# Kernel tuning notes

Measured on AMD Instinct MI355X. Metric: run time of the kernel, lower is better.

Reference implementation:

```python
import jax, jax.numpy as jnp
import numpy as np

N = 50000      # nodes
E = 800000     # edges (before self-loops)
F_IN = 128     # num_features
HID = 32       # hidden_channels
HEADS = 4
CLS = 40       # num_classes
NEG_SLOPE = 0.2


def setup_inputs() -> dict:
    key = jax.random.key(0)
    ks = jax.random.split(key, 10)
    s = 0.1
    x = jax.random.normal(ks[0], (N, F_IN), jnp.float32)
    edge_index = jax.random.randint(ks[1], (2, E), 0, N, jnp.int32)
    W1 = jax.random.normal(ks[2], (F_IN, HEADS * HID), jnp.float32) * s
    att_src1 = jax.random.normal(ks[3], (HEADS, HID), jnp.float32) * s
    att_dst1 = jax.random.normal(ks[4], (HEADS, HID), jnp.float32) * s
    b1 = jnp.zeros((HEADS * HID,), jnp.float32)
    W2 = jax.random.normal(ks[5], (HEADS * HID, CLS), jnp.float32) * s
    att_src2 = jax.random.normal(ks[6], (1, CLS), jnp.float32) * s
    att_dst2 = jax.random.normal(ks[7], (1, CLS), jnp.float32) * s
    b2 = jnp.zeros((CLS,), jnp.float32)
    return {"x": x, "edge_index": edge_index,
            "W1": W1, "att_src1": att_src1, "att_dst1": att_dst1, "b1": b1,
            "W2": W2, "att_src2": att_src2, "att_dst2": att_dst2, "b2": b2}


def gat_layer(x, src, dst, W, a_src, a_dst, b, concat):
    """PyG GATConv: per-head linear, edge attention logits a_src.h_j + a_dst.h_i,
    LeakyReLU, segment softmax over incoming edges per dst, weighted scatter-sum."""
    n = x.shape[0]
    H, C = a_src.shape
    h = (x @ W).reshape(n, H, C)                       # [N, H, C]
    al_s = jnp.einsum('nhc,hc->nh', h, a_src)          # [N, H]
    al_d = jnp.einsum('nhc,hc->nh', h, a_dst)          # [N, H]
    e = jax.nn.leaky_relu(al_s[src] + al_d[dst], NEG_SLOPE)  # [E, H]
    e_max = jax.lax.stop_gradient(jax.ops.segment_max(e, dst, num_segments=n))
    e = jnp.exp(e - e_max[dst])
    denom = jax.ops.segment_sum(e, dst, num_segments=n)      # [N, H]
    alpha = e / (denom[dst] + 1e-16)                         # [E, H]
    out = jax.ops.segment_sum(h[src] * alpha[:, :, None], dst, num_segments=n)  # [N, H, C]
    out = out.reshape(n, H * C) if concat else out.mean(axis=1)
    return out + b


def reference(x, edge_index, W1, att_src1, att_dst1, b1, W2, att_src2, att_dst2, b2):
    n = x.shape[0]
    loops = jnp.arange(n, dtype=edge_index.dtype)
    src = jnp.concatenate([edge_index[0], loops])  # PyG adds self-loops by default
    dst = jnp.concatenate([edge_index[1], loops])
    h = gat_layer(x, src, dst, W1, att_src1, att_dst1, b1, concat=True)
    h = jax.nn.relu(h)  # dropout is identity in eval mode
    h = gat_layer(h, src, dst, W2, att_src2, att_dst2, b2, concat=False)
    return jax.nn.log_softmax(h, axis=1)
```

## Files before the change

### kernel.cpp

```cpp
#include <hip/hip_runtime.h>
#include <hip/hip_bf16.h>
#include <cstdint>
#include <cstddef>

#define NN 50000
#define EE 800000
#define ETOT (EE + NN)
#define FIN 128
#define D1 128
#define HEADS 4
#define HID 32
#define CLS 40
#define NEG 0.2f
#define MAXDEG 64
#define NPART 8
#define PSIZE 6250
#define GB 79
#define BGB (NPART * GB)

typedef __attribute__((ext_vector_type(8))) short short8;
typedef __attribute__((ext_vector_type(4))) float float4v;

union U16 { uint4 u; short8 s; };

__device__ __forceinline__ float bf2f(unsigned short u) {
    union { unsigned int i; float f; } v; v.i = ((unsigned int)u) << 16; return v.f;
}
__device__ __forceinline__ unsigned short f2bf(float f) {
    union { unsigned int i; float f; } v; v.f = f;
    unsigned int r = v.i + 0x7fffu + ((v.i >> 16) & 1u);
    return (unsigned short)(r >> 16);
}

__global__ __launch_bounds__(256, 4) void bg_k(const int* __restrict__ eidx,
                                               int* __restrict__ cnt,
                                               unsigned short* __restrict__ ssrcp,
                                               const float* __restrict__ X,
                                               const float* __restrict__ W,
                                               const float* __restrict__ as1,
                                               const float* __restrict__ ad1,
                                               unsigned int* __restrict__ H1b,
                                               float* __restrict__ ALS1,
                                               float* __restrict__ ALD1) {
    __shared__ uint4 Wl[2048];
    __shared__ float sas[128], sad[128];
    int t = threadIdx.x;

    if (blockIdx.x < BGB) {
        int part = blockIdx.x & (NPART - 1);
        int g    = blockIdx.x >> 3;
        int lo = part * PSIZE, hi = lo + PSIZE;
        int stride = GB * 256;
        for (int n = lo + g * 256 + t; n < hi; n += stride) {
            int slot = atomicAdd(&cnt[n], 1);
            if (slot < MAXDEG) ssrcp[n * MAXDEG + slot] = (unsigned short)n;
        }
        const int4* dst4 = (const int4*)(eidx + EE);
        for (int i4 = g * 256 + t; i4 < EE / 4; i4 += stride) {
            int4 d = dst4[i4];
            int base = i4 * 4;
            if (d.x >= lo && d.x < hi) {
                int sN = eidx[base];
                int slot = atomicAdd(&cnt[d.x], 1);
                if (slot < MAXDEG) ssrcp[d.x * MAXDEG + slot] = (unsigned short)sN;
            }
            if (d.y >= lo && d.y < hi) {
                int sN = eidx[base + 1];
                int slot = atomicAdd(&cnt[d.y], 1);
                if (slot < MAXDEG) ssrcp[d.y * MAXDEG + slot] = (unsigned short)sN;
            }
            if (d.z >= lo && d.z < hi) {
                int sN = eidx[base + 2];
                int slot = atomicAdd(&cnt[d.z], 1);
                if (slot < MAXDEG) ssrcp[d.z * MAXDEG + slot] = (unsigned short)sN;
            }
            if (d.w >= lo && d.w < hi) {
                int sN = eidx[base + 3];
                int slot = atomicAdd(&cnt[d.w], 1);
                if (slot < MAXDEG) ssrcp[d.w * MAXDEG + slot] = (unsigned short)sN;
            }
        }
        return;
    }

    int bI = blockIdx.x - BGB;
    if (t < 128) { sas[t] = as1[t]; sad[t] = ad1[t]; }
    for (int g = t; g < 2048; g += 256) {
        int ct = g >> 8, rem = g & 255, kc = rem >> 6, l = rem & 63;
        int c = ct * 16 + (l & 15);
        int k0 = kc * 32 + (l >> 4) * 8;
        U16 u;
#pragma unroll
        for (int j = 0; j < 8; j++) u.s[j] = (short)f2bf(W[(k0 + j) * D1 + c]);
        Wl[g] = u.u;
    }
    __syncthreads();

    int wid = t >> 6, lane = t & 63, quad = lane >> 4, lrow = lane & 15;
    int wrow0 = bI * 128 + wid * 32;

    short8 afr[2][4];
#pragma unroll
    for (int rt = 0; rt < 2; rt++) {
        int r = wrow0 + rt * 16 + lrow;
#pragma unroll
        for (int kc = 0; kc < 4; kc++) {
            short8 a = {0, 0, 0, 0, 0, 0, 0, 0};
            if (r < NN) {
                const float* xp = X + (size_t)r * FIN + kc * 32 + quad * 8;
                float4 x0 = *(const float4*)xp;
                float4 x1 = *(const float4*)(xp + 4);
                a[0] = (short)f2bf(x0.x); a[1] = (short)f2bf(x0.y);
                a[2] = (short)f2bf(x0.z); a[3] = (short)f2bf(x0.w);
                a[4] = (short)f2bf(x1.x); a[5] = (short)f2bf(x1.y);
                a[6] = (short)f2bf(x1.z); a[7] = (short)f2bf(x1.w);
            }
            afr[rt][kc] = a;
        }
    }

    float4v acc[2][4];

    for (int cp = 0; cp < 2; ++cp) {
#pragma unroll
        for (int rt = 0; rt < 2; rt++)
#pragma unroll
            for (int c4 = 0; c4 < 4; c4++) acc[rt][c4] = (float4v)(0.f);

#pragma unroll
        for (int c4 = 0; c4 < 4; c4++) {
#pragma unroll
            for (int kc = 0; kc < 4; kc++) {
                U16 b; b.u = Wl[((cp * 4 + c4) * 4 + kc) * 64 + lane];
                acc[0][c4] = __builtin_amdgcn_mfma_f32_16x16x32_bf16(afr[0][kc], b.s, acc[0][c4], 0, 0, 0);
                acc[1][c4] = __builtin_amdgcn_mfma_f32_16x16x32_bf16(afr[1][kc], b.s, acc[1][c4], 0, 0, 0);
            }
        }

#pragma unroll
        for (int rt = 0; rt < 2; rt++) {
#pragma unroll
            for (int reg = 0; reg < 4; reg++) {
                float ps[2] = {0.f, 0.f};
                float pd[2] = {0.f, 0.f};
#pragma unroll
                for (int c4 = 0; c4 < 4; c4++) {
                    float v = acc[rt][c4][reg];
                    int ct = cp * 4 + c4;
                    ps[c4 >> 1] += v * sas[ct * 16 + lrow];
                    pd[c4 >> 1] += v * sad[ct * 16 + lrow];
                }
#pragma unroll
                for (int o = 1; o < 16; o <<= 1) {
#pragma unroll
                    for (int h = 0; h < 2; h++) {
                        ps[h] += __shfl_xor(ps[h], o);
                        pd[h] += __shfl_xor(pd[h], o);
                    }
                }
                int r = wrow0 + rt * 16 + quad * 4 + reg;
                if (lrow == 0 && r < NN) {
                    *(float2*)&ALS1[(size_t)r * 4 + cp * 2] = make_float2(ps[0], ps[1]);
                    *(float2*)&ALD1[(size_t)r * 4 + cp * 2] = make_float2(pd[0], pd[1]);
                }
            }
        }

#pragma unroll
        for (int rt = 0; rt < 2; rt++)
#pragma unroll
            for (int c4 = 0; c4 < 4; c4++)
#pragma unroll
                for (int reg = 0; reg < 4; reg++) {
                    float v = acc[rt][c4][reg];
                    float o = __shfl_xor(v, 1);
                    int r = wrow0 + rt * 16 + quad * 4 + reg;
                    if (((lane & 1) == 0) && r < NN) {
                        unsigned int u = (unsigned int)f2bf(v) | ((unsigned int)f2bf(o) << 16);
                        H1b[(size_t)r * 64 + (cp * 4 + c4) * 8 + (lrow >> 1)] = u;
                    }
                }
    }
}

__global__ __launch_bounds__(256) void gather1_k(const int* __restrict__ cnt,
                                                 const unsigned short* __restrict__ ssrcp,
                                                 const uint4* __restrict__ H1b4,
                                                 const float4* __restrict__ ALS,
                                                 const float4* __restrict__ ALD,
                                                 const float* __restrict__ b1,
                                                 uint4* __restrict__ OUT1b4) {
    __shared__ float wlds[4][MAXDEG][4];
    __shared__ int sidlds[4][MAXDEG];
    int wid = threadIdx.x >> 6, lane = threadIdx.x & 63;
    int v = blockIdx.x * 4 + wid;
    int deg = min(cnt[v], MAXDEG);
    float4 ad = ALD[v];
    float w0 = 0.f, w1 = 0.f, w2 = 0.f, w3 = 0.f;
    if (lane < deg) {
        int s = (int)ssrcp[v * MAXDEG + lane];
        sidlds[wid][lane] = s;
        float4 as = ALS[s];
        float l0 = as.x + ad.x; l0 = l0 > 0.f ? l0 : NEG * l0;
        float l1 = as.y + ad.y; l1 = l1 > 0.f ? l1 : NEG * l1;
        float l2 = as.z + ad.z; l2 = l2 > 0.f ? l2 : NEG * l2;
        float l3 = as.w + ad.w; l3 = l3 > 0.f ? l3 : NEG * l3;
        w0 = __expf(l0); w1 = __expf(l1); w2 = __expf(l2); w3 = __expf(l3);
        wlds[wid][lane][0] = w0; wlds[wid][lane][1] = w1;
        wlds[wid][lane][2] = w2; wlds[wid][lane][3] = w3;
    }
    float d0 = w0, d1 = w1, d2 = w2, d3 = w3;
#pragma unroll
    for (int o = 1; o < 64; o <<= 1) {
        d0 += __shfl_xor(d0, o); d1 += __shfl_xor(d1, o);
        d2 += __shfl_xor(d2, o); d3 += __shfl_xor(d3, o);
    }
    __syncthreads();
    int g = lane >> 4, l = lane & 15, head = l >> 2;
    float a0=0.f,a1=0.f,a2=0.f,a3=0.f,a4=0.f,a5=0.f,a6=0.f,a7=0.f;
    {
        int j = g;
        bool valid = j < deg;
        float wj = 0.f; uint4 q = {};
        if (valid) {
            wj = wlds[wid][j][head];
            q = H1b4[(size_t)sidlds[wid][j] * 16 + l];
        }
        while (valid) {
            int jn = j + 4;
            bool vn = jn < deg;
            float wn = 0.f; uint4 qn = {};
            if (vn) {
                wn = wlds[wid][jn][head];
                qn = H1b4[(size_t)sidlds[wid][jn] * 16 + l];
            }
            a0 += wj * bf2f((unsigned short)(q.x & 0xffffu));
            a1 += wj * bf2f((unsigned short)(q.x >> 16));
            a2 += wj * bf2f((unsigned short)(q.y & 0xffffu));
            a3 += wj * bf2f((unsigned short)(q.y >> 16));
            a4 += wj * bf2f((unsigned short)(q.z & 0xffffu));
            a5 += wj * bf2f((unsigned short)(q.z >> 16));
            a6 += wj * bf2f((unsigned short)(q.w & 0xffffu));
            a7 += wj * bf2f((unsigned short)(q.w >> 16));
            j = jn; valid = vn; wj = wn; q = qn;
        }
    }
#pragma unroll
    for (int o = 16; o < 64; o <<= 1) {
        a0 += __shfl_xor(a0, o); a1 += __shfl_xor(a1, o);
        a2 += __shfl_xor(a2, o); a3 += __shfl_xor(a3, o);
        a4 += __shfl_xor(a4, o); a5 += __shfl_xor(a5, o);
        a6 += __shfl_xor(a6, o); a7 += __shfl_xor(a7, o);
    }
    if (lane < 16) {
        float den = (head == 0) ? d0 : (head == 1) ? d1 : (head == 2) ? d2 : d3;
        den += 1e-16f;
        float4 bA = *(const float4*)&b1[8 * l];
        float4 bB = *(const float4*)&b1[8 * l + 4];
        float o0 = fmaxf(a0 / den + bA.x, 0.f);
        float o1 = fmaxf(a1 / den + bA.y, 0.f);
        float o2 = fmaxf(a2 / den + bA.z, 0.f);
        float o3 = fmaxf(a3 / den + bA.w, 0.f);
        float o4 = fmaxf(a4 / den + bB.x, 0.f);
        float o5 = fmaxf(a5 / den + bB.y, 0.f);
        float o6 = fmaxf(a6 / den + bB.z, 0.f);
        float o7 = fmaxf(a7 / den + bB.w, 0.f);
        uint4 u;
        u.x = (unsigned int)f2bf(o0) | ((unsigned int)f2bf(o1) << 16);
        u.y = (unsigned int)f2bf(o2) | ((unsigned int)f2bf(o3) << 16);
        u.z = (unsigned int)f2bf(o4) | ((unsigned int)f2bf(o5) << 16);
        u.w = (unsigned int)f2bf(o6) | ((unsigned int)f2bf(o7) << 16);
        OUT1b4[(size_t)v * 16 + l] = u;
    }
}

__global__ __launch_bounds__(256) void gemm2_k(const unsigned int* __restrict__ OUT1b,
                                               const float* __restrict__ W2,
                                               const float* __restrict__ as2,
                                               const float* __restrict__ ad2,
                                               unsigned int* __restrict__ H2b,
                                               float* __restrict__ ALS2,
                                               float* __restrict__ ALD2) {
    __shared__ uint4 Wl[768];
    __shared__ float sas[48], sad[48];
    int t = threadIdx.x;
    if (t < 48) {
        sas[t] = (t < CLS) ? as2[t] : 0.f;
        sad[t] = (t < CLS) ? ad2[t] : 0.f;
    }
    for (int g = t; g < 768; g += 256) {
        int ct = g >> 8, rem = g & 255, kc = rem >> 6, l = rem & 63;
        int c = ct * 16 + (l & 15);
        int k0 = kc * 32 + (l >> 4) * 8;
        U16 u;
#pragma unroll
        for (int j = 0; j < 8; j++)
            u.s[j] = (c < CLS) ? (short)f2bf(W2[(k0 + j) * CLS + c]) : (short)0;
        Wl[g] = u.u;
    }
    __syncthreads();

    int wid = t >> 6, lane = t & 63, quad = lane >> 4, lrow = lane & 15;
    int wrow0 = blockIdx.x * 128 + wid * 32;

    U16 afr[2][4];
#pragma unroll
    for (int rt = 0; rt < 2; rt++) {
        int r = wrow0 + rt * 16 + lrow;
#pragma unroll
        for (int kc = 0; kc < 4; kc++) {
            if (r < NN)
                afr[rt][kc].u = ((const uint4*)OUT1b)[(size_t)r * 16 + kc * 4 + quad];
            else
                afr[rt][kc].u = make_uint4(0, 0, 0, 0);
        }
    }

    float4v acc[2][3];
#pragma unroll
    for (int rt = 0; rt < 2; rt++)
#pragma unroll
        for (int ct = 0; ct < 3; ct++) acc[rt][ct] = (float4v)(0.f);

#pragma unroll
    for (int ct = 0; ct < 3; ct++) {
#pragma unroll
        for (int kc = 0; kc < 4; kc++) {
            U16 b; b.u = Wl[(ct * 4 + kc) * 64 + lane];
            acc[0][ct] = __builtin_amdgcn_mfma_f32_16x16x32_bf16(afr[0][kc].s, b.s, acc[0][ct], 0, 0, 0);
            acc[1][ct] = __builtin_amdgcn_mfma_f32_16x16x32_bf16(afr[1][kc].s, b.s, acc[1][ct], 0, 0, 0);
        }
    }

#pragma unroll
    for (int rt = 0; rt < 2; rt++) {
#pragma unroll
        for (int reg = 0; reg < 4; reg++) {
            float ps = 0.f, pd = 0.f;
#pragma unroll
            for (int ct = 0; ct < 3; ct++) {
                float v = acc[rt][ct][reg];
                ps += v * sas[ct * 16 + lrow];
                pd += v * sad[ct * 16 + lrow];
            }
#pragma unroll
            for (int o = 1; o < 16; o <<= 1) {
                ps += __shfl_xor(ps, o);
                pd += __shfl_xor(pd, o);
            }
            int r = wrow0 + rt * 16 + quad * 4 + reg;
            if (lrow == 0 && r < NN) {
                ALS2[r] = ps;
                ALD2[r] = pd;
            }
        }
    }

#pragma unroll
    for (int rt = 0; rt < 2; rt++)
#pragma unroll
        for (int ct = 0; ct < 3; ct++)
#pragma unroll
            for (int reg = 0; reg < 4; reg++) {
                float v = acc[rt][ct][reg];
                float o = __shfl_xor(v, 1);
                int r = wrow0 + rt * 16 + quad * 4 + reg;
                int c = ct * 16 + lrow;
                if (((lane & 1) == 0) && c < CLS && r < NN) {
                    unsigned int u = (unsigned int)f2bf(v) | ((unsigned int)f2bf(o) << 16);
                    H2b[(size_t)r * 20 + (c >> 1)] = u;
                }
            }
}

__global__ __launch_bounds__(256) void gather2_k(const int* __restrict__ cnt,
                                                 const unsigned short* __restrict__ ssrcp,
                                                 const unsigned int* __restrict__ H2b,
                                                 const float* __restrict__ ALS,
                                                 const float* __restrict__ ALD,
                                                 const float* __restrict__ b2,
                                                 float* __restrict__ out) {
    int wid = threadIdx.x >> 6, t = threadIdx.x & 63;
    int v = blockIdx.x * 4 + wid;
    int deg = min(cnt[v], MAXDEG);
    __shared__ float w[4][MAXDEG];
    __shared__ int sid[4][MAXDEG];
    __shared__ float part[4][3][CLS];
    float den = 0.f;
    float adv = ALD[v];
    if (t < deg) {
        int s = (int)ssrcp[(size_t)v * MAXDEG + t];
        sid[wid][t] = s;
        float l = ALS[s] + adv; l = l > 0.f ? l : NEG * l;
        float e = __expf(l);
        w[wid][t] = e; den = e;
    }
    __syncthreads();
    int g = t / 20, c = t % 20;
    if (t < 60) {
        float ax = 0.f, ay = 0.f;
        int j = g;
        bool valid = j < deg;
        float wj = 0.f; unsigned int u = 0u;
        if (valid) { wj = w[wid][j]; u = H2b[(size_t)sid[wid][j] * 20 + c]; }
        while (valid) {
            int jn = j + 3;
            bool vn = jn < deg;
            float wn = 0.f; unsigned int un = 0u;
            if (vn) { wn = w[wid][jn]; un = H2b[(size_t)sid[wid][jn] * 20 + c]; }
            ax += wj * bf2f((unsigned short)(u & 0xffffu));
            ay += wj * bf2f((unsigned short)(u >> 16));
            j = jn; valid = vn; wj = wn; u = un;
        }
        part[wid][g][2 * c] = ax;
        part[wid][g][2 * c + 1] = ay;
    }
#pragma unroll
    for (int o = 32; o > 0; o >>= 1) den += __shfl_xor(den, o);
    __syncthreads();
    float z = (t < CLS) ? (part[wid][0][t] + part[wid][1][t] + part[wid][2][t]) / (den + 1e-16f) + b2[t]
                        : -1e30f;
    float mx = z;
#pragma unroll
    for (int o = 32; o > 0; o >>= 1) mx = fmaxf(mx, __shfl_xor(mx, o));
    float ex = (t < CLS) ? __expf(z - mx) : 0.f;
    float se = ex;
#pragma unroll
    for (int o = 32; o > 0; o >>= 1) se += __shfl_xor(se, o);
    if (t < CLS) out[(size_t)v * CLS + t] = z - mx - __logf(se);
}

extern "C" void kernel_launch(void* const* d_in, const int* in_sizes, int n_in,
                              void* d_out, int out_size, void* d_ws, size_t ws_size,
                              hipStream_t stream) {
    const float* x   = (const float*)d_in[0];
    const int*   eix = (const int*)d_in[1];
    const float* W1  = (const float*)d_in[2];
    const float* as1 = (const float*)d_in[3];
    const float* ad1 = (const float*)d_in[4];
    const float* b1  = (const float*)d_in[5];
    const float* W2  = (const float*)d_in[6];
    const float* as2 = (const float*)d_in[7];
    const float* ad2 = (const float*)d_in[8];
    const float* b2  = (const float*)d_in[9];
    float* out = (float*)d_out;

    char* p = (char*)d_ws;
    auto carve = [&](size_t bytes) -> void* {
        void* r = (void*)p;
        p += (bytes + 255) & ~(size_t)255;
        return r;
    };
    unsigned int* H1b   = (unsigned int*)carve((size_t)NN * 64 * 4);
    unsigned int* OUT1b = (unsigned int*)carve((size_t)NN * 64 * 4);
    unsigned int* H2b   = (unsigned int*)carve((size_t)NN * 20 * 4);
    float* ALS1 = (float*)carve((size_t)NN * 4 * 4);
    float* ALD1 = (float*)carve((size_t)NN * 4 * 4);
    float* ALS2 = (float*)carve((size_t)NN * 4);
    float* ALD2 = (float*)carve((size_t)NN * 4);
    int* cnt    = (int*)carve((size_t)NN * 4);
    unsigned short* ssrcp = (unsigned short*)carve((size_t)NN * MAXDEG * 2);

    hipMemsetAsync(cnt, 0, (size_t)NN * 4, stream);

    int gemmBlocks = (NN + 127) / 128;
    bg_k<<<BGB + gemmBlocks, 256, 0, stream>>>(eix, cnt, ssrcp, x, W1, as1, ad1,
                                               H1b, ALS1, ALD1);
    gather1_k<<<NN / 4, 256, 0, stream>>>(cnt, ssrcp, (const uint4*)H1b,
                                          (const float4*)ALS1, (const float4*)ALD1,
                                          b1, (uint4*)OUT1b);
    gemm2_k<<<(NN + 127) / 128, 256, 0, stream>>>(OUT1b, W2, as2, ad2, H2b, ALS2, ALD2);
    gather2_k<<<NN / 4, 256, 0, stream>>>(cnt, ssrcp, H2b, ALS2, ALD2, b2, out);
}
```

Before: 219.4 us.

## Replace global-atomic edge bucketing with per-block LDS histogram partitions

Edge bucketing by destination now uses 64 blocks. Each owns a contiguous node range and counts slots with shared-memory atomics instead of global atomics on cnt, then writes the final counts out, so the memset is removed. Shared memory is unioned with the GEMM staging buffers. In exchange, every partition block scans the full destination array, which multiplies edge reads and concentrates work on fewer blocks.

Result: slower. 819.5 us (+273.5%).

```diff
diff --git a/kernel.cpp b/kernel.cpp
--- a/kernel.cpp
+++ b/kernel.cpp
@@ -5,7 +5,6 @@
 
 #define NN 50000
 #define EE 800000
-#define ETOT (EE + NN)
 #define FIN 128
 #define D1 128
 #define HEADS 4
@@ -13,10 +12,9 @@
 #define CLS 40
 #define NEG 0.2f
 #define MAXDEG 64
-#define NPART 8
-#define PSIZE 6250
-#define GB 79
-#define BGB (NPART * GB)
+#define PBLK 64
+#define PSZ 782
+#define GEMM1B 391
 
 typedef __attribute__((ext_vector_type(8))) short short8;
 typedef __attribute__((ext_vector_type(4))) float float4v;
@@ -31,6 +29,11 @@
     unsigned int r = v.i + 0x7fffu + ((v.i >> 16) & 1u);
     return (unsigned short)(r >> 16);
 }
+
+union BSM {
+    struct { uint4 Wl[2048]; float sas[128]; float sad[128]; } g;
+    int hist[PSZ];
+};
 
 __global__ __launch_bounds__(256, 4) void bg_k(const int* __restrict__ eidx,
                                                int* __restrict__ cnt,
@@ -42,49 +45,46 @@
                                                unsigned int* __restrict__ H1b,
                                                float* __restrict__ ALS1,
                                                float* __restrict__ ALD1) {
-    __shared__ uint4 Wl[2048];
-    __shared__ float sas[128], sad[128];
+    __shared__ BSM sm;
     int t = threadIdx.x;
 
-    if (blockIdx.x < BGB) {
-        int part = blockIdx.x & (NPART - 1);
-        int g    = blockIdx.x >> 3;
-        int lo = part * PSIZE, hi = lo + PSIZE;
-        int stride = GB * 256;
-        for (int n = lo + g * 256 + t; n < hi; n += stride) {
-            int slot = atomicAdd(&cnt[n], 1);
-            if (slot < MAXDEG) ssrcp[n * MAXDEG + slot] = (unsigned short)n;
-        }
+    if (blockIdx.x < PBLK) {
+        int lo = blockIdx.x * PSZ;
+        int hi = min(lo + PSZ, NN);
+        int n = hi - lo;
+        for (int i = t; i < n; i += 256) {
+            sm.hist[i] = 1;
+            ssrcp[(size_t)(lo + i) * MAXDEG] = (unsigned short)(lo + i);
+        }
+        __syncthreads();
         const int4* dst4 = (const int4*)(eidx + EE);
-        for (int i4 = g * 256 + t; i4 < EE / 4; i4 += stride) {
+        for (int i4 = t; i4 < EE / 4; i4 += 256) {
             int4 d = dst4[i4];
             int base = i4 * 4;
             if (d.x >= lo && d.x < hi) {
-                int sN = eidx[base];
-                int slot = atomicAdd(&cnt[d.x], 1);
-                if (slot < MAXDEG) ssrcp[d.x * MAXDEG + slot] = (unsigned short)sN;
+                int s = atomicAdd(&sm.hist[d.x - lo], 1);
+                if (s < MAXDEG) ssrcp[(size_t)d.x * MAXDEG + s] = (unsigned short)eidx[base];
             }
             if (d.y >= lo && d.y < hi) {
-                int sN = eidx[base + 1];
-                int slot = atomicAdd(&cnt[d.y], 1);
-                if (slot < MAXDEG) ssrcp[d.y * MAXDEG + slot] = (unsigned short)sN;
+                int s = atomicAdd(&sm.hist[d.y - lo], 1);
+                if (s < MAXDEG) ssrcp[(size_t)d.y * MAXDEG + s] = (unsigned short)eidx[base + 1];
             }
             if (d.z >= lo && d.z < hi) {
-                int sN = eidx[base + 2];
-                int slot = atomicAdd(&cnt[d.z], 1);
-                if (slot < MAXDEG) ssrcp[d.z * MAXDEG + slot] = (unsigned short)sN;
+                int s = atomicAdd(&sm.hist[d.z - lo], 1);
+                if (s < MAXDEG) ssrcp[(size_t)d.z * MAXDEG + s] = (unsigned short)eidx[base + 2];
             }
             if (d.w >= lo && d.w < hi) {
-                int sN = eidx[base + 3];
-                int slot = atomicAdd(&cnt[d.w], 1);
-                if (slot < MAXDEG) ssrcp[d.w * MAXDEG + slot] = (unsigned short)sN;
-            }
-        }
+                int s = atomicAdd(&sm.hist[d.w - lo], 1);
+                if (s < MAXDEG) ssrcp[(size_t)d.w * MAXDEG + s] = (unsigned short)eidx[base + 3];
+            }
+        }
+        __syncthreads();
+        for (int i = t; i < n; i += 256) cnt[lo + i] = sm.hist[i];
         return;
     }
 
-    int bI = blockIdx.x - BGB;
-    if (t < 128) { sas[t] = as1[t]; sad[t] = ad1[t]; }
+    int bI = blockIdx.x - PBLK;
+    if (t < 128) { sm.g.sas[t] = as1[t]; sm.g.sad[t] = ad1[t]; }
     for (int g = t; g < 2048; g += 256) {
         int ct = g >> 8, rem = g & 255, kc = rem >> 6, l = rem & 63;
         int c = ct * 16 + (l & 15);
@@ -92,7 +92,7 @@
         U16 u;
 #pragma unroll
         for (int j = 0; j < 8; j++) u.s[j] = (short)f2bf(W[(k0 + j) * D1 + c]);
-        Wl[g] = u.u;
+        sm.g.Wl[g] = u.u;
     }
     __syncthreads();
 
@@ -131,7 +131,7 @@
         for (int c4 = 0; c4 < 4; c4++) {
 #pragma unroll
             for (int kc = 0; kc < 4; kc++) {
-                U16 b; b.u = Wl[((cp * 4 + c4) * 4 + kc) * 64 + lane];
+                U16 b; b.u = sm.g.Wl[((cp * 4 + c4) * 4 + kc) * 64 + lane];
                 acc[0][c4] = __builtin_amdgcn_mfma_f32_16x16x32_bf16(afr[0][kc], b.s, acc[0][c4], 0, 0, 0);
                 acc[1][c4] = __builtin_amdgcn_mfma_f32_16x16x32_bf16(afr[1][kc], b.s, acc[1][c4], 0, 0, 0);
             }
@@ -147,8 +147,8 @@
                 for (int c4 = 0; c4 < 4; c4++) {
                     float v = acc[rt][c4][reg];
                     int ct = cp * 4 + c4;
-                    ps[c4 >> 1] += v * sas[ct * 16 + lrow];
-                    pd[c4 >> 1] += v * sad[ct * 16 + lrow];
+                    ps[c4 >> 1] += v * sm.g.sas[ct * 16 + lrow];
+                    pd[c4 >> 1] += v * sm.g.sad[ct * 16 + lrow];
                 }
 #pragma unroll
                 for (int o = 1; o < 16; o <<= 1) {
@@ -198,7 +198,7 @@
     float4 ad = ALD[v];
     float w0 = 0.f, w1 = 0.f, w2 = 0.f, w3 = 0.f;
     if (lane < deg) {
-        int s = (int)ssrcp[v * MAXDEG + lane];
+        int s = (int)ssrcp[(size_t)v * MAXDEG + lane];
         sidlds[wid][lane] = s;
         float4 as = ALS[s];
         float l0 = as.x + ad.x; l0 = l0 > 0.f ? l0 : NEG * l0;
@@ -461,11 +461,9 @@
     int* cnt    = (int*)carve((size_t)NN * 4);
     unsigned short* ssrcp = (unsigned short*)carve((size_t)NN * MAXDEG * 2);
 
-    hipMemsetAsync(cnt, 0, (size_t)NN * 4, stream);
-
-    int gemmBlocks = (NN + 127) / 128;
-    bg_k<<<BGB + gemmBlocks, 256, 0, stream>>>(eix, cnt, ssrcp, x, W1, as1, ad1,
-                                               H1b, ALS1, ALD1);
+
+    bg_k<<<PBLK + GEMM1B, 256, 0, stream>>>(eix, cnt, ssrcp, x, W1, as1, ad1,
+                                            H1b, ALS1, ALD1);
     gather1_k<<<NN / 4, 256, 0, stream>>>(cnt, ssrcp, (const uint4*)H1b,
                                           (const float4*)ALS1, (const float4*)ALD1,
                                           b1, (uint4*)OUT1b);
```
